# Kernel optimization log

Measured on AMD Instinct MI355X. Metric: run time of the kernel, lower is better.

The kernel has to match this reference:

```python
import jax, jax.numpy as jnp
import numpy as np
from jax import lax

NUM_CLASSES = 19
B, H, W = 4, 512, 512
IGNORE = 255
BLOCK = 16
MAX_N_RATIO = 0.01
LB_SMOOTH = 0.2
MAX_CLIP_DIST = 20.0
BORDER_FACTOR = 0.1
MAX_DIS = 1e5

# ---------- setup helpers (numpy, exact EDT matching scipy distance_transform_edt) ----------

def _edt(mask):
    """Exact Euclidean distance to nearest True pixel. mask: (H,W) bool."""
    Hm, Wm = mask.shape
    INF = 1e6
    g = np.where(mask, 0.0, INF).astype(np.float32)
    for j in range(1, Wm):
        g[:, j] = np.minimum(g[:, j], g[:, j - 1] + 1.0)
    for j in range(Wm - 2, -1, -1):
        g[:, j] = np.minimum(g[:, j], g[:, j + 1] + 1.0)
    gg = g * g  # (H,W) squared 1D row distances
    rows = np.arange(Hm, dtype=np.float32)
    out = np.empty((Hm, Wm), np.float32)
    CH = 64
    for s in range(0, Hm, CH):
        d2 = (rows[s:s + CH, None] - rows[None, :]) ** 2  # (CH,H)
        out[s:s + CH] = np.sqrt(np.min(d2[:, :, None] + gg[None, :, :], axis=1))
    return out


def _dist_maps(targets):
    """Replicates gtruth2boundary + dist_map_transform + relu(-dist): relu(EDT_to_boundary - 1)."""
    t = targets[:, 0]
    ud = np.zeros(t.shape, bool)
    lr = np.zeros(t.shape, bool)
    ud[:, :-1] = (t[:, 1:] - t[:, :-1]) != 0
    lr[:, :, :-1] = (t[:, :, 1:] - t[:, :, :-1]) != 0
    bnd = ud | lr | (t == IGNORE)
    out = np.zeros(t.shape, np.float32)
    for i in range(t.shape[0]):
        if bnd[i].any():
            out[i] = np.maximum(_edt(bnd[i]) - 1.0, 0.0)
    return out[:, None]  # (B,1,H,W)


def setup_inputs():
    key = jax.random.key(0)
    k1, k2 = jax.random.split(key)
    slices = jax.random.normal(k1, (B, NUM_CLASSES, H, W), jnp.float32)
    low = np.asarray(jax.random.randint(k2, (B, 1, H // BLOCK, W // BLOCK), 0, NUM_CLASSES))
    tgt = np.repeat(np.repeat(low, BLOCK, 2), BLOCK, 3).astype(np.int32)
    dist_maps = jnp.asarray(_dist_maps(tgt))
    return {"slices": slices, "dist_maps": dist_maps, "targets": jnp.asarray(tgt)}


# neighbor offset order from the torch code; index 8 is the center
_DX = [1, -1, 0, 0, -1, 1, -1, 1, 0]
_DY = [0, 0, -1, 1, 1, 1, -1, -1, 0]


def reference(slices, dist_maps, targets):
    Bc, C, Hc, Wc = slices.shape
    x = jnp.transpose(slices, (0, 2, 3, 1))               # (B,H,W,C)
    lsm = jax.nn.log_softmax(x, axis=-1)
    sm = jnp.exp(lsm)

    # ---- slices2boundary: per-pixel KL between adjacent pixels ----
    kl_ud = jnp.sum(sm[:, :-1] * (lsm[:, :-1] - lsm[:, 1:]), axis=-1)      # (B,H-1,W)
    kl_ud = jnp.pad(kl_ud, ((0, 0), (0, 1), (0, 0)))
    kl_lr = jnp.sum(sm[:, :, :-1] * (lsm[:, :, :-1] - lsm[:, :, 1:]), axis=-1)
    kl_lr = jnp.pad(kl_lr, ((0, 0), (0, 0), (0, 1)))
    klc = lax.stop_gradient(kl_ud + kl_lr)                # threshold is non-differentiable anyway

    max_N = Hc * Wc * MAX_N_RATIO
    eps = lax.while_loop(lambda e: jnp.sum(klc > e) > max_N,
                         lambda e: e * jnp.float32(1.2),
                         jnp.float32(1e-5))
    kb = (klc > eps).astype(jnp.float32)[:, None]          # (B,1,H,W)
    k3 = jnp.ones((1, 1, 3, 3), jnp.float32)
    dil = lax.conv_general_dilated(kb, k3, (1, 1), 'SAME',
                                   dimension_numbers=('NCHW', 'OIHW', 'NCHW'))
    pb = dil[:, 0] > 0                                     # pred boundary (B,H,W) bool

    # ---- get_orientation (dense masked version of the nonzero/gather code) ----
    pd = jnp.pad(dist_maps[:, 0], ((0, 0), (1, 1), (1, 1)), constant_values=MAX_DIS)
    lsm_p = lax.stop_gradient(jnp.pad(lsm, ((0, 0), (1, 1), (1, 1), (0, 0)), mode='edge'))
    sm_p = lax.stop_gradient(jnp.pad(sm, ((0, 0), (1, 1), (1, 1), (0, 0)), mode='edge'))

    dists, kls = [], []
    for dx, dy in zip(_DX, _DY):
        dists.append(pd[:, 1 + dx:1 + dx + Hc, 1 + dy:1 + dy + Wc])
        if dx != 0 or dy != 0:
            l_s = lsm_p[:, 1 + dx:1 + dx + Hc, 1 + dy:1 + dy + Wc]
            s_s = sm_p[:, 1 + dx:1 + dx + Hc, 1 + dy:1 + dy + Wc]
            # kl_div(center, neighbor) = softmax(nb) * (log_softmax(nb) - log_softmax(center))
            kls.append(jnp.sum(s_s * (l_s - lsm), axis=-1))
    dist9 = jnp.stack(dists, axis=-1)                      # (B,H,W,9)
    kl8 = jnp.stack(kls, axis=-1)                          # (B,H,W,8)

    dgt = jnp.argmin(dist9, axis=-1)                       # direction ground truth 0..8
    valid = pb & (dgt != 8)

    # label-smoothed softmax CE over the 8 directions (pytorch-loss LSSCE V1 semantics)
    lb_pos = 1.0 - LB_SMOOTH
    lb_neg = LB_SMOOTH / 8.0
    logq = jax.nn.log_softmax(kl8, axis=-1)
    onehot = jax.nn.one_hot(jnp.clip(dgt, 0, 7), 8, dtype=logq.dtype)
    smooth_lab = onehot * lb_pos + (1.0 - onehot) * lb_neg
    lsce = -jnp.sum(logq * smooth_lab, axis=-1)            # (B,H,W)

    w = jnp.minimum(dist_maps[:, 0], MAX_CLIP_DIST) / MAX_CLIP_DIST
    vm = valid.astype(jnp.float32)
    border_loss = jnp.sum(lsce * vm) * jnp.sum(w * vm)
    border_loss = jnp.where(jnp.sum(pb) > 1, border_loss, jnp.float32(0.0))

    # ---- target cross-entropy (reduction='none' then .sum()) ----
    tgt = targets[:, 0]
    ce = -jnp.take_along_axis(lsm, jnp.clip(tgt, 0, C - 1)[..., None], axis=-1)[..., 0]
    ce = jnp.where(tgt == IGNORE, 0.0, ce)
    target_loss = jnp.sum(ce)

    return BORDER_FACTOR * border_loss + target_loss
```

## Files before the change

kernel.cpp:

```cpp
#include <hip/hip_runtime.h>


#define NCLS 19
#define HH 512
#define WW 512
#define HWC (HH*WW)
#define CHW (NCLS*HWC)
#define NPIX (4*HWC)
#define NEPS 256
#define MAXDIS 100000.0f
#define LIST_CAP 32768
#define CNT_THRESH 2621u
#define SEG 4

#define O_LSE   0u
#define O_KLC   4194304u
#define O_TL    8388608u
#define O_CNT   8421376u
#define O_HIST  8425472u
#define O_LISTN 8426500u
#define O_SUMS  8426512u
#define O_LIST  8426532u
#define MEMSET_OFF O_HIST
#define MEMSET_LEN 1056u

__global__ __launch_bounds__(256, 4) void kF_fused(
    const float* __restrict__ x, const int* __restrict__ tgt,
    float* __restrict__ lse_g, float* __restrict__ klc,
    unsigned int* __restrict__ hist, double* __restrict__ tl_part) {
  __shared__ float eps[NEPS];
  __shared__ unsigned int lh[NEPS + 1];
  __shared__ double sdce[256];
  int tid = threadIdx.x;
  for (int i = tid; i < NEPS + 1; i += 256) lh[i] = 0u;
  if (tid == 0) {
    float e = 1e-5f;
    for (int i = 0; i < NEPS; i++) { eps[i] = e; e *= 1.2f; }
  }
  __syncthreads();

  int bid = blockIdx.x;
  int b = bid >> 8;
  int r = bid & 255;
  int wh = r >> 7;
  int seg = r & 127;
  int h0 = seg * SEG;
  int w = (wh << 8) + tid;
  const float* xb = x + (size_t)b * CHW + w;
  int pbase = b * HWC + w;
  bool hasR = (w < WW - 1);
  int offR = hasR ? 1 : 0;
  bool edge = ((tid & 63) == 63);

  float cur[NCLS];
  {
    const float* x0 = xb + h0 * WW;
#pragma unroll
    for (int c = 0; c < NCLS; c++) cur[c] = x0[(size_t)c * HWC];
  }
  float lse_cur;
  {
    float m = -1e30f;
#pragma unroll
    for (int c = 0; c < NCLS; c++) m = fmaxf(m, cur[c]);
    float s = 0.f;
#pragma unroll
    for (int c = 0; c < NCLS; c++) s += __expf(cur[c] - m);
    lse_cur = m + __logf(s);
  }
  double ce_acc = 0.0;

  for (int h = h0; h < h0 + SEG; ++h) {
    int p = pbase + h * WW;
    int row_n = (h < HH - 1) ? h + 1 : HH - 1;
    const float* xn = xb + row_n * WW;
    float nxt[NCLS];
#pragma unroll
    for (int c = 0; c < NCLS; c++) nxt[c] = xn[(size_t)c * HWC];

    float xr[NCLS];
#pragma unroll
    for (int c = 0; c < NCLS; c++) xr[c] = __shfl_down(cur[c], 1);
    float lse_r = __shfl_down(lse_cur, 1);
    if (edge) {
      const float* xc_ptr = xb + h * WW;
#pragma unroll
      for (int c = 0; c < NCLS; c++) xr[c] = xc_ptr[(size_t)c * HWC + offR];
      float m = -1e30f;
#pragma unroll
      for (int c = 0; c < NCLS; c++) m = fmaxf(m, xr[c]);
      float s = 0.f;
#pragma unroll
      for (int c = 0; c < NCLS; c++) s += __expf(xr[c] - m);
      lse_r = m + __logf(s);
    }

    int t = tgt[p];
    if (t != 255) {
      float xt = cur[0];
#pragma unroll
      for (int c = 1; c < NCLS; c++) xt = (t == c) ? cur[c] : xt;
      ce_acc += (double)(lse_cur - xt);
    }

    float lse_nxt;
    {
      float m = -1e30f;
#pragma unroll
      for (int c = 0; c < NCLS; c++) m = fmaxf(m, nxt[c]);
      float s = 0.f;
#pragma unroll
      for (int c = 0; c < NCLS; c++) s += __expf(nxt[c] - m);
      lse_nxt = m + __logf(s);
    }

    bool hasD = (h < HH - 1);
    float sD = 0.f, sR = 0.f;
#pragma unroll
    for (int c = 0; c < NCLS; c++) {
      float lmc = cur[c] - lse_cur;
      float pc = __expf(lmc);
      sD += pc * (lmc - (nxt[c] - lse_nxt));
      sR += pc * (lmc - (xr[c] - lse_r));
    }
    float kv = (hasD ? sD : 0.f) + (hasR ? sR : 0.f);
    klc[p] = kv;
    lse_g[p] = lse_cur;

    int lo = 0, hi = NEPS;
    while (lo < hi) {
      int mid = (lo + hi) >> 1;
      if (kv > eps[mid]) lo = mid + 1; else hi = mid;
    }
    atomicAdd(&lh[lo], 1u);

#pragma unroll
    for (int c = 0; c < NCLS; c++) cur[c] = nxt[c];
    lse_cur = lse_nxt;
  }

  sdce[tid] = ce_acc;
  __syncthreads();
  for (int o = 128; o > 0; o >>= 1) {
    if (tid < o) sdce[tid] += sdce[tid + o];
    __syncthreads();
  }
  if (tid == 0) tl_part[bid] = sdce[0];
  for (int i = tid; i < NEPS + 1; i += 256)
    if (lh[i]) atomicAdd(&hist[i], lh[i]);
}

__global__ void kD1_compact(const float* __restrict__ klc, const unsigned int* __restrict__ hist,
                            int* __restrict__ list, unsigned int* __restrict__ list_n,
                            unsigned int* __restrict__ cnt_part) {
  __shared__ unsigned int shist[257];
  __shared__ float seps;
  __shared__ unsigned int lcnt, lbase;
  __shared__ int lbuf[1024];
  int tid = threadIdx.x;
  for (int i = tid; i < 257; i += 256) shist[i] = hist[i];
  if (tid == 0) lcnt = 0u;
  __syncthreads();
  if (tid == 0) {
    unsigned int cnt = 0;
    for (int i = 1; i <= NEPS; i++) cnt += shist[i];
    int K = 0;
    while (cnt > CNT_THRESH && K < NEPS - 1) {
      K++;
      cnt -= shist[K];
    }
    float e = 1e-5f;
    for (int i = 0; i < K; i++) e *= 1.2f;
    seps = e;
  }
  __syncthreads();
  float eps = seps;
  int base = blockIdx.x * 1024;
#pragma unroll
  for (int k = 0; k < 4; k++) {
    int p = base + k * 256 + tid;
    int b = p >> 18;
    int hw = p & (HWC - 1);
    int h = hw >> 9;
    int w = hw & 511;
    const float* kb = klc + b * HWC;
    bool pb = false;
#pragma unroll
    for (int dh = -1; dh <= 1; dh++)
#pragma unroll
      for (int dw = -1; dw <= 1; dw++) {
        int hh = h + dh, wn = w + dw;
        if (hh >= 0 && hh < HH && wn >= 0 && wn < WW)
          pb = pb || (kb[hh * WW + wn] > eps);
      }
    if (pb) {
      unsigned int idx = atomicAdd(&lcnt, 1u);
      lbuf[idx] = p;
    }
  }
  __syncthreads();
  if (tid == 0) {
    unsigned int c = lcnt;
    lbase = c ? atomicAdd(list_n, c) : 0u;
    cnt_part[blockIdx.x] = c;
  }
  __syncthreads();
  unsigned int c = lcnt, bo = lbase;
  for (unsigned int j = tid; j < c; j += 256) {
    unsigned int dst = bo + j;
    if (dst < LIST_CAP) list[dst] = lbuf[j];
  }
}

__global__ __launch_bounds__(256, 4) void kD2_border(
    const float* __restrict__ x, const float* __restrict__ lse,
    const float* __restrict__ dist, const int* __restrict__ list,
    const unsigned int* __restrict__ list_n,
    double* __restrict__ sums ) {
  const int DXc[9] = {1, -1, 0, 0, -1, 1, -1, 1, 0};
  const int DYc[9] = {0, 0, -1, 1, 1, 1, -1, -1, 0};
  __shared__ float skl[32][8];
  __shared__ float swl[4], sww[4];
  int tid = threadIdx.x;
  int gid = blockIdx.x * 256 + tid;
  int i = gid >> 3, k = gid & 7;
  unsigned int n = *list_n;
  if (n > LIST_CAP) n = LIST_CAP;
  float lsce = 0.f, wv = 0.f;
  bool act = (i < (int)n);
  int g = 8;
  float d8c = 0.f;
  int p = 0, b = 0, h = 0, w = 0, hw = 0;
  if (act) {
    p = list[i];
    b = p >> 18;
    hw = p & (HWC - 1);
    h = hw >> 9;
    w = hw & 511;
    const float* db = dist + b * HWC;
    float dv[9];
#pragma unroll
    for (int kk = 0; kk < 9; kk++) {
      int hh = h + DXc[kk], wn = w + DYc[kk];
      dv[kk] = (hh >= 0 && hh < HH && wn >= 0 && wn < WW) ? db[hh * WW + wn] : MAXDIS;
    }
    float dmin = dv[0];
    g = 0;
#pragma unroll
    for (int kk = 1; kk < 9; kk++)
      if (dv[kk] < dmin) { dmin = dv[kk]; g = kk; }
    d8c = dv[8];
    if (g != 8) {
      int dx = ((34898 >> (2 * k)) & 3) - 1;
      int dy = ((2693  >> (2 * k)) & 3) - 1;
      int hh = min(max(h + dx, 0), HH - 1);
      int wn = min(max(w + dy, 0), WW - 1);
      int hwn = hh * WW + wn;
      const float* xp = x + (size_t)b * CHW;
      float ln = lse[b * HWC + hwn];
      float lc = lse[p];
      float xnv[NCLS], xcv[NCLS];
#pragma unroll
      for (int c = 0; c < NCLS; c++) xnv[c] = xp[(size_t)c * HWC + hwn];
#pragma unroll
      for (int c = 0; c < NCLS; c++) xcv[c] = xp[(size_t)c * HWC + hw];
      float s = 0.f;
#pragma unroll
      for (int c = 0; c < NCLS; c++) {
        float lsn = xnv[c] - ln;
        s += __expf(lsn) * (lsn - (xcv[c] - lc));
      }
      skl[tid >> 3][k] = s;
    }
  }
  __syncthreads();
  if (act && g != 8 && k == 0) {
    float kl8[8];
#pragma unroll
    for (int kk = 0; kk < 8; kk++) kl8[kk] = skl[tid >> 3][kk];
    float m8 = kl8[0];
#pragma unroll
    for (int kk = 1; kk < 8; kk++) m8 = fmaxf(m8, kl8[kk]);
    float se = 0.f;
#pragma unroll
    for (int kk = 0; kk < 8; kk++) se += __expf(kl8[kk] - m8);
    float l8 = m8 + __logf(se);
    float sum_lq = 0.f, lq_g = 0.f;
#pragma unroll
    for (int kk = 0; kk < 8; kk++) {
      float lq = kl8[kk] - l8;
      sum_lq += lq;
      if (kk == g) lq_g = lq;
    }
    lsce = -(0.025f * sum_lq + 0.775f * lq_g);
    wv = fminf(d8c, 20.0f) * (1.0f / 20.0f);
  }
  float rl = lsce, rw = wv;
#pragma unroll
  for (int o = 32; o > 0; o >>= 1) {
    rl += __shfl_xor(rl, o);
    rw += __shfl_xor(rw, o);
  }
  if ((tid & 63) == 0) { swl[tid >> 6] = rl; sww[tid >> 6] = rw; }
  __syncthreads();
  if (tid == 0) {
    float tl = swl[0] + swl[1] + swl[2] + swl[3];
    float tw = sww[0] + sww[1] + sww[2] + sww[3];
    if (tl != 0.f || tw != 0.f) {
      atomicAdd(&sums[0], (double)tl);
      atomicAdd(&sums[1], (double)tw);
    }
  }
}

__global__ void kE_final(const double* __restrict__ tl_part, const unsigned int* __restrict__ cnt_part,
                         const double* __restrict__ sums, float* __restrict__ out) {
  __shared__ double sd[256];
  __shared__ unsigned int su[256];
  int t = threadIdx.x;
  double a = 0.0;
  for (int i = t; i < 1024; i += 256) a += tl_part[i];
  sd[t] = a;
  unsigned int c = 0;
  for (int i = t; i < 1024; i += 256) c += cnt_part[i];
  su[t] = c;
  __syncthreads();
  for (int o = 128; o > 0; o >>= 1) {
    if (t < o) { sd[t] += sd[t + o]; su[t] += su[t + o]; }
    __syncthreads();
  }
  if (t == 0) {
    double border = (su[0] > 1u) ? sums[0] * sums[1] : 0.0;
    out[0] = (float)(0.1 * border + sd[0]);
  }
}

extern "C" void kernel_launch(void* const* d_in, const int* in_sizes, int n_in,
                              void* d_out, int out_size, void* d_ws, size_t ws_size,
                              hipStream_t stream) {
  const float* x    = (const float*)d_in[0];
  const float* dist = (const float*)d_in[1];
  const int*   tgt  = (const int*)d_in[2];
  float* out = (float*)d_out;

  char* ws = (char*)d_ws;
  float*        lse      = (float*)(ws + O_LSE);
  float*        klc      = (float*)(ws + O_KLC);
  double*       tl_part  = (double*)(ws + O_TL);
  unsigned int* cnt_part = (unsigned int*)(ws + O_CNT);
  unsigned int* hist     = (unsigned int*)(ws + O_HIST);
  unsigned int* list_n   = (unsigned int*)(ws + O_LISTN);
  double*       sums     = (double*)(ws + O_SUMS);
  int*          list     = (int*)(ws + O_LIST);

  hipMemsetAsync(ws + MEMSET_OFF, 0, MEMSET_LEN, stream);

  kF_fused<<<1024, 256, 0, stream>>>(x, tgt, lse, klc, hist, tl_part);
  kD1_compact<<<NPIX / 1024, 256, 0, stream>>>(klc, hist, list, list_n, cnt_part);
  kD2_border<<<(LIST_CAP * 8) / 256, 256, 0, stream>>>(x, lse, dist, list, list_n, sums);
  kE_final<<<1, 256, 0, stream>>>(tl_part, cnt_part, sums, out);
}
```

Measured before the change: 192.7 us.

## Process two pixels per thread with float2 loads and fold final reduction into border kernel

The fused kernel now gives each thread two adjacent columns over two rows, using float2 vector loads for logits, targets and outputs. The right-neighbour KL for the first pixel is computed from registers, and only the second pixel needs a cross-lane shuffle. The separate single-block final kernel is removed and replaced by a last-block-done counter inside the border kernel, which saves one launch. In exchange the kernel holds more live registers (two 19-class arrays each for the current and next rows) and adds threadfence and atomic ordering logic.

```diff
diff --git a/kernel.cpp b/kernel.cpp
--- a/kernel.cpp
+++ b/kernel.cpp
@@ -11,7 +11,6 @@
 #define MAXDIS 100000.0f
 #define LIST_CAP 32768
 #define CNT_THRESH 2621u
-#define SEG 4
 
 #define O_LSE   0u
 #define O_KLC   4194304u
@@ -20,9 +19,10 @@
 #define O_HIST  8425472u
 #define O_LISTN 8426500u
 #define O_SUMS  8426512u
-#define O_LIST  8426532u
+#define O_CTR   8426528u
+#define O_LIST  8426536u
 #define MEMSET_OFF O_HIST
-#define MEMSET_LEN 1056u
+#define MEMSET_LEN 1060u
 
 __global__ __launch_bounds__(256, 4) void kF_fused(
     const float* __restrict__ x, const int* __restrict__ tgt,
@@ -41,102 +41,130 @@
 
   int bid = blockIdx.x;
   int b = bid >> 8;
-  int r = bid & 255;
-  int wh = r >> 7;
-  int seg = r & 127;
-  int h0 = seg * SEG;
-  int w = (wh << 8) + tid;
-  const float* xb = x + (size_t)b * CHW + w;
-  int pbase = b * HWC + w;
-  bool hasR = (w < WW - 1);
-  int offR = hasR ? 1 : 0;
-  bool edge = ((tid & 63) == 63);
-
-  float cur[NCLS];
+  int seg = bid & 255;
+  int h0 = seg * 2;
+  int w0 = tid * 2;
+  const float* xb = x + (size_t)b * CHW + w0;
+  int pbase = b * HWC + w0;
+  bool edge = ((tid & 63) == 63) && (tid != 255);
+  bool hasR1 = (tid != 255);
+
+  float cur0[NCLS], cur1[NCLS];
   {
     const float* x0 = xb + h0 * WW;
 #pragma unroll
-    for (int c = 0; c < NCLS; c++) cur[c] = x0[(size_t)c * HWC];
-  }
-  float lse_cur;
+    for (int c = 0; c < NCLS; c++) {
+      float2 v = *reinterpret_cast<const float2*>(x0 + (size_t)c * HWC);
+      cur0[c] = v.x; cur1[c] = v.y;
+    }
+  }
+  float lse_cur0, lse_cur1;
   {
-    float m = -1e30f;
-#pragma unroll
-    for (int c = 0; c < NCLS; c++) m = fmaxf(m, cur[c]);
-    float s = 0.f;
-#pragma unroll
-    for (int c = 0; c < NCLS; c++) s += __expf(cur[c] - m);
-    lse_cur = m + __logf(s);
+    float m0 = -1e30f, m1 = -1e30f;
+#pragma unroll
+    for (int c = 0; c < NCLS; c++) { m0 = fmaxf(m0, cur0[c]); m1 = fmaxf(m1, cur1[c]); }
+    float s0 = 0.f, s1 = 0.f;
+#pragma unroll
+    for (int c = 0; c < NCLS; c++) { s0 += __expf(cur0[c] - m0); s1 += __expf(cur1[c] - m1); }
+    lse_cur0 = m0 + __logf(s0);
+    lse_cur1 = m1 + __logf(s1);
   }
   double ce_acc = 0.0;
 
-  for (int h = h0; h < h0 + SEG; ++h) {
+  for (int h = h0; h < h0 + 2; ++h) {
     int p = pbase + h * WW;
     int row_n = (h < HH - 1) ? h + 1 : HH - 1;
     const float* xn = xb + row_n * WW;
-    float nxt[NCLS];
-#pragma unroll
-    for (int c = 0; c < NCLS; c++) nxt[c] = xn[(size_t)c * HWC];
-
-    float xr[NCLS];
-#pragma unroll
-    for (int c = 0; c < NCLS; c++) xr[c] = __shfl_down(cur[c], 1);
-    float lse_r = __shfl_down(lse_cur, 1);
+    float nxt0[NCLS], nxt1[NCLS];
+#pragma unroll
+    for (int c = 0; c < NCLS; c++) {
+      float2 v = *reinterpret_cast<const float2*>(xn + (size_t)c * HWC);
+      nxt0[c] = v.x; nxt1[c] = v.y;
+    }
+
+    int2 tp = *reinterpret_cast<const int2*>(tgt + p);
+    if (tp.x != 255) {
+      float xt = cur0[0];
+#pragma unroll
+      for (int c = 1; c < NCLS; c++) xt = (tp.x == c) ? cur0[c] : xt;
+      ce_acc += (double)(lse_cur0 - xt);
+    }
+    if (tp.y != 255) {
+      float xt = cur1[0];
+#pragma unroll
+      for (int c = 1; c < NCLS; c++) xt = (tp.y == c) ? cur1[c] : xt;
+      ce_acc += (double)(lse_cur1 - xt);
+    }
+
+    float lse_nxt0, lse_nxt1;
+    {
+      float m0 = -1e30f, m1 = -1e30f;
+#pragma unroll
+      for (int c = 0; c < NCLS; c++) { m0 = fmaxf(m0, nxt0[c]); m1 = fmaxf(m1, nxt1[c]); }
+      float s0 = 0.f, s1 = 0.f;
+#pragma unroll
+      for (int c = 0; c < NCLS; c++) { s0 += __expf(nxt0[c] - m0); s1 += __expf(nxt1[c] - m1); }
+      lse_nxt0 = m0 + __logf(s0);
+      lse_nxt1 = m1 + __logf(s1);
+    }
+
+    bool hasD = (h < HH - 1);
+    float sD0 = 0.f, sR0 = 0.f;
+#pragma unroll
+    for (int c = 0; c < NCLS; c++) {
+      float lmc = cur0[c] - lse_cur0;
+      float pc = __expf(lmc);
+      sD0 += pc * (lmc - (nxt0[c] - lse_nxt0));
+      sR0 += pc * (lmc - (cur1[c] - lse_cur1));
+    }
+    float lse_r1 = __shfl_down(lse_cur0, 1);
+    float sD1 = 0.f, sR1 = 0.f;
+#pragma unroll
+    for (int c = 0; c < NCLS; c++) {
+      float xr = __shfl_down(cur0[c], 1);
+      float lmc = cur1[c] - lse_cur1;
+      float pc = __expf(lmc);
+      sD1 += pc * (lmc - (nxt1[c] - lse_nxt1));
+      sR1 += pc * (lmc - (xr - lse_r1));
+    }
     if (edge) {
-      const float* xc_ptr = xb + h * WW;
-#pragma unroll
-      for (int c = 0; c < NCLS; c++) xr[c] = xc_ptr[(size_t)c * HWC + offR];
+      float xrE[NCLS];
+#pragma unroll
+      for (int c = 0; c < NCLS; c++) xrE[c] = xb[h * WW + (size_t)c * HWC + 2];
       float m = -1e30f;
 #pragma unroll
-      for (int c = 0; c < NCLS; c++) m = fmaxf(m, xr[c]);
+      for (int c = 0; c < NCLS; c++) m = fmaxf(m, xrE[c]);
       float s = 0.f;
 #pragma unroll
-      for (int c = 0; c < NCLS; c++) s += __expf(xr[c] - m);
-      lse_r = m + __logf(s);
-    }
-
-    int t = tgt[p];
-    if (t != 255) {
-      float xt = cur[0];
-#pragma unroll
-      for (int c = 1; c < NCLS; c++) xt = (t == c) ? cur[c] : xt;
-      ce_acc += (double)(lse_cur - xt);
-    }
-
-    float lse_nxt;
-    {
-      float m = -1e30f;
-#pragma unroll
-      for (int c = 0; c < NCLS; c++) m = fmaxf(m, nxt[c]);
-      float s = 0.f;
-#pragma unroll
-      for (int c = 0; c < NCLS; c++) s += __expf(nxt[c] - m);
-      lse_nxt = m + __logf(s);
-    }
-
-    bool hasD = (h < HH - 1);
-    float sD = 0.f, sR = 0.f;
-#pragma unroll
-    for (int c = 0; c < NCLS; c++) {
-      float lmc = cur[c] - lse_cur;
-      float pc = __expf(lmc);
-      sD += pc * (lmc - (nxt[c] - lse_nxt));
-      sR += pc * (lmc - (xr[c] - lse_r));
-    }
-    float kv = (hasD ? sD : 0.f) + (hasR ? sR : 0.f);
-    klc[p] = kv;
-    lse_g[p] = lse_cur;
+      for (int c = 0; c < NCLS; c++) s += __expf(xrE[c] - m);
+      float lse_rE = m + __logf(s);
+      sR1 = 0.f;
+#pragma unroll
+      for (int c = 0; c < NCLS; c++) {
+        float lmc = cur1[c] - lse_cur1;
+        float pc = __expf(lmc);
+        sR1 += pc * (lmc - (xrE[c] - lse_rE));
+      }
+    }
+    float kv0 = (hasD ? sD0 : 0.f) + sR0;
+    float kv1 = (hasD ? sD1 : 0.f) + (hasR1 ? sR1 : 0.f);
+
+    float2 kvp; kvp.x = kv0; kvp.y = kv1;
+    *reinterpret_cast<float2*>(klc + p) = kvp;
+    float2 lsp; lsp.x = lse_cur0; lsp.y = lse_cur1;
+    *reinterpret_cast<float2*>(lse_g + p) = lsp;
 
     int lo = 0, hi = NEPS;
-    while (lo < hi) {
-      int mid = (lo + hi) >> 1;
-      if (kv > eps[mid]) lo = mid + 1; else hi = mid;
-    }
+    while (lo < hi) { int mid = (lo + hi) >> 1; if (kv0 > eps[mid]) lo = mid + 1; else hi = mid; }
     atomicAdd(&lh[lo], 1u);
-
-#pragma unroll
-    for (int c = 0; c < NCLS; c++) cur[c] = nxt[c];
-    lse_cur = lse_nxt;
+    lo = 0; hi = NEPS;
+    while (lo < hi) { int mid = (lo + hi) >> 1; if (kv1 > eps[mid]) lo = mid + 1; else hi = mid; }
+    atomicAdd(&lh[lo], 1u);
+
+#pragma unroll
+    for (int c = 0; c < NCLS; c++) { cur0[c] = nxt0[c]; cur1[c] = nxt1[c]; }
+    lse_cur0 = lse_nxt0;
+    lse_cur1 = lse_nxt1;
   }
 
   sdce[tid] = ce_acc;
@@ -216,11 +244,16 @@
     const float* __restrict__ x, const float* __restrict__ lse,
     const float* __restrict__ dist, const int* __restrict__ list,
     const unsigned int* __restrict__ list_n,
-    double* __restrict__ sums ) {
+    double* __restrict__ sums ,
+    const double* __restrict__ tl_part, const unsigned int* __restrict__ cnt_part,
+    unsigned int* __restrict__ ctr, float* __restrict__ out) {
   const int DXc[9] = {1, -1, 0, 0, -1, 1, -1, 1, 0};
   const int DYc[9] = {0, 0, -1, 1, 1, 1, -1, -1, 0};
   __shared__ float skl[32][8];
   __shared__ float swl[4], sww[4];
+  __shared__ int islast;
+  __shared__ double sd[256];
+  __shared__ unsigned int su[256];
   int tid = threadIdx.x;
   int gid = blockIdx.x * 256 + tid;
   int i = gid >> 3, k = gid & 7;
@@ -310,28 +343,30 @@
       atomicAdd(&sums[0], (double)tl);
       atomicAdd(&sums[1], (double)tw);
     }
-  }
-}
-
-__global__ void kE_final(const double* __restrict__ tl_part, const unsigned int* __restrict__ cnt_part,
-                         const double* __restrict__ sums, float* __restrict__ out) {
-  __shared__ double sd[256];
-  __shared__ unsigned int su[256];
-  int t = threadIdx.x;
-  double a = 0.0;
-  for (int i = t; i < 1024; i += 256) a += tl_part[i];
-  sd[t] = a;
-  unsigned int c = 0;
-  for (int i = t; i < 1024; i += 256) c += cnt_part[i];
-  su[t] = c;
-  __syncthreads();
-  for (int o = 128; o > 0; o >>= 1) {
-    if (t < o) { sd[t] += sd[t + o]; su[t] += su[t + o]; }
+    __threadfence();
+    unsigned int old = atomicAdd(ctr, 1u);
+    islast = (old == gridDim.x - 1) ? 1 : 0;
+  }
+  __syncthreads();
+  if (islast) {
+    __threadfence();
+    double a = 0.0;
+    for (int j = tid; j < 1024; j += 256) a += tl_part[j];
+    sd[tid] = a;
+    unsigned int c = 0;
+    for (int j = tid; j < 1024; j += 256) c += cnt_part[j];
+    su[tid] = c;
     __syncthreads();
-  }
-  if (t == 0) {
-    double border = (su[0] > 1u) ? sums[0] * sums[1] : 0.0;
-    out[0] = (float)(0.1 * border + sd[0]);
+    for (int o = 128; o > 0; o >>= 1) {
+      if (tid < o) { sd[tid] += sd[tid + o]; su[tid] += su[tid + o]; }
+      __syncthreads();
+    }
+    if (tid == 0) {
+      double s0 = atomicAdd(&sums[0], 0.0);
+      double s1 = atomicAdd(&sums[1], 0.0);
+      double border = (su[0] > 1u) ? s0 * s1 : 0.0;
+      out[0] = (float)(0.1 * border + sd[0]);
+    }
   }
 }
 
@@ -351,12 +386,13 @@
   unsigned int* hist     = (unsigned int*)(ws + O_HIST);
   unsigned int* list_n   = (unsigned int*)(ws + O_LISTN);
   double*       sums     = (double*)(ws + O_SUMS);
+  unsigned int* ctr      = (unsigned int*)(ws + O_CTR);
   int*          list     = (int*)(ws + O_LIST);
 
   hipMemsetAsync(ws + MEMSET_OFF, 0, MEMSET_LEN, stream);
 
   kF_fused<<<1024, 256, 0, stream>>>(x, tgt, lse, klc, hist, tl_part);
   kD1_compact<<<NPIX / 1024, 256, 0, stream>>>(klc, hist, list, list_n, cnt_part);
-  kD2_border<<<(LIST_CAP * 8) / 256, 256, 0, stream>>>(x, lse, dist, list, list_n, sums);
-  kE_final<<<1, 256, 0, stream>>>(tl_part, cnt_part, sums, out);
+  kD2_border<<<(LIST_CAP * 8) / 256, 256, 0, stream>>>(x, lse, dist, list, list_n, sums,
+                                                       tl_part, cnt_part, ctr, out);
 }
```

Result: slower. 227.2 us (+17.9%).
